# Optimization experiments

Measured on AMD Instinct MI355X. Metric: run time of the kernel, lower is better.

Reference implementation:

```python
import jax, jax.numpy as jnp
import numpy as np

D = 256; NH = 8; NLEV = 4; NPTS = 4; DH = D // NH
DFFN = 1024; B = 8; LQ = 900
SHAPES = np.array([[100, 100], [50, 50], [25, 25], [13, 13]], dtype=np.int64)
STARTS = np.concatenate([[0], np.cumsum(SHAPES[:, 0] * SHAPES[:, 1])[:-1]]).astype(np.int64)
LEN = int((SHAPES[:, 0] * SHAPES[:, 1]).sum())


def _ln(x, w, b, eps=1e-5):
    m = x.mean(-1, keepdims=True)
    v = ((x - m) ** 2).mean(-1, keepdims=True)
    return (x - m) / jnp.sqrt(v + eps) * w + b


def _msdeform(q, ref, src, val_w, val_b, off_w, off_b, aw_w, aw_b, op_w, op_b):
    # Multi-scale deformable attention (Deformable DETR core), grid_sample
    # bilinear / zeros padding / align_corners=False semantics.
    Bq, Lq = q.shape[0], q.shape[1]
    value = (src @ val_w + val_b).reshape(Bq, -1, NH, DH)
    off = (q @ off_w + off_b).reshape(Bq, Lq, NH, NLEV, NPTS, 2)
    aw = jax.nn.softmax((q @ aw_w + aw_b).reshape(Bq, Lq, NH, NLEV * NPTS), -1)
    aw = aw.reshape(Bq, Lq, NH, NLEV, NPTS)
    norm = jnp.asarray(SHAPES[:, ::-1].copy(), dtype=q.dtype)  # (W_l, H_l)
    loc = ref[:, :, None, :, None, :] + off / norm[None, None, None, :, None, :]
    out = jnp.zeros((Bq, Lq, NH, DH), q.dtype)
    for l in range(NLEV):
        Hl, Wl = int(SHAPES[l, 0]), int(SHAPES[l, 1]); s = int(STARTS[l])
        v = value[:, s:s + Hl * Wl]                  # [B, Hl*Wl, NH, DH]
        lx = loc[:, :, :, l, :, 0] * Wl - 0.5        # align_corners=False pixel coords
        ly = loc[:, :, :, l, :, 1] * Hl - 0.5        # [B, Lq, NH, NPTS]
        x0 = jnp.floor(lx); y0 = jnp.floor(ly)
        fx = lx - x0; fy = ly - y0
        x0 = x0.astype(jnp.int32); y0 = y0.astype(jnp.int32)
        samp = jnp.zeros((Bq, Lq, NH, NPTS, DH), q.dtype)
        for dx, dy in ((0, 0), (1, 0), (0, 1), (1, 1)):
            xi = x0 + dx; yi = y0 + dy
            w = (fx if dx else 1.0 - fx) * (fy if dy else 1.0 - fy)
            valid = (xi >= 0) & (xi < Wl) & (yi >= 0) & (yi < Hl)
            idx = jnp.clip(yi, 0, Hl - 1) * Wl + jnp.clip(xi, 0, Wl - 1)
            idx_f = idx.transpose(0, 1, 3, 2).reshape(Bq, Lq * NPTS, NH)
            g = jnp.take_along_axis(v, idx_f[..., None], axis=1)
            g = g.reshape(Bq, Lq, NPTS, NH, DH).transpose(0, 1, 3, 2, 4)
            samp = samp + jnp.where(valid, w, 0.0)[..., None] * g
        out = out + jnp.sum(samp * aw[:, :, :, l, :, None], axis=3)
    return out.reshape(Bq, Lq, D) @ op_w + op_b


def _forward(tgt, query_pos, reference_points, src, qkv_w, qkv_b, out_w, out_b,
             ln2_w, ln2_b, val_w, val_b, off_w, off_b, aw_w, aw_b, op_w, op_b,
             ln1_w, ln1_b, w1, b1, w2, b2, ln3_w, ln3_b):
    Bq, Lq, _ = tgt.shape
    # --- self attention: q=k=tgt+pos, value=tgt (eval mode, no dropout) ---
    q = tgt + query_pos
    wq, wk, wv = qkv_w[:, :D], qkv_w[:, D:2 * D], qkv_w[:, 2 * D:]
    bq, bk, bv = qkv_b[:D], qkv_b[D:2 * D], qkv_b[2 * D:]
    qh = (q @ wq + bq).reshape(Bq, Lq, NH, DH)
    kh = (q @ wk + bk).reshape(Bq, Lq, NH, DH)
    vh = (tgt @ wv + bv).reshape(Bq, Lq, NH, DH)
    scores = jnp.einsum('bqhd,bkhd->bhqk', qh, kh) / jnp.sqrt(jnp.asarray(DH, tgt.dtype))
    attn = jax.nn.softmax(scores, -1)
    sa = jnp.einsum('bhqk,bkhd->bqhd', attn, vh).reshape(Bq, Lq, D) @ out_w + out_b
    tgt = _ln(tgt + sa, ln2_w, ln2_b)
    # --- multi-scale deformable cross attention ---
    ca = _msdeform(tgt + query_pos, reference_points, src,
                   val_w, val_b, off_w, off_b, aw_w, aw_b, op_w, op_b)
    tgt = _ln(tgt + ca, ln1_w, ln1_b)
    # --- FFN ---
    ff = jax.nn.relu(tgt @ w1 + b1) @ w2 + b2
    return _ln(tgt + ff, ln3_w, ln3_b)


def setup_inputs():
    key = jax.random.key(0)
    ks = jax.random.split(key, 16)
    s = 0.02
    return {
        'tgt': jax.random.normal(ks[0], (B, LQ, D), jnp.float32),
        'query_pos': jax.random.normal(ks[1], (B, LQ, D), jnp.float32),
        'reference_points': jax.random.uniform(ks[2], (B, LQ, NLEV, 2), jnp.float32),
        'src': jax.random.normal(ks[3], (B, LEN, D), jnp.float32),
        'spatial_shapes': jnp.asarray(SHAPES),
        'level_start_index': jnp.asarray(STARTS),
        'qkv_w': jax.random.normal(ks[4], (D, 3 * D), jnp.float32) * s,
        'qkv_b': jnp.zeros((3 * D,), jnp.float32),
        'out_w': jax.random.normal(ks[5], (D, D), jnp.float32) * s,
        'out_b': jnp.zeros((D,), jnp.float32),
        'ln2_w': jnp.ones((D,), jnp.float32), 'ln2_b': jnp.zeros((D,), jnp.float32),
        'val_w': jax.random.normal(ks[6], (D, D), jnp.float32) * s,
        'val_b': jnp.zeros((D,), jnp.float32),
        'off_w': jax.random.normal(ks[7], (D, NH * NLEV * NPTS * 2), jnp.float32) * s,
        'off_b': jax.random.normal(ks[8], (NH * NLEV * NPTS * 2,), jnp.float32) * 0.5,
        'aw_w': jax.random.normal(ks[9], (D, NH * NLEV * NPTS), jnp.float32) * s,
        'aw_b': jnp.zeros((NH * NLEV * NPTS,), jnp.float32),
        'op_w': jax.random.normal(ks[10], (D, D), jnp.float32) * s,
        'op_b': jnp.zeros((D,), jnp.float32),
        'ln1_w': jnp.ones((D,), jnp.float32), 'ln1_b': jnp.zeros((D,), jnp.float32),
        'w1': jax.random.normal(ks[11], (D, DFFN), jnp.float32) * s,
        'b1': jnp.zeros((DFFN,), jnp.float32),
        'w2': jax.random.normal(ks[12], (DFFN, D), jnp.float32) * s,
        'b2': jnp.zeros((D,), jnp.float32),
        'ln3_w': jnp.ones((D,), jnp.float32), 'ln3_b': jnp.zeros((D,), jnp.float32),
    }


def reference(tgt, query_pos, reference_points, src, spatial_shapes, level_start_index,
              qkv_w, qkv_b, out_w, out_b, ln2_w, ln2_b, val_w, val_b, off_w, off_b,
              aw_w, aw_b, op_w, op_b, ln1_w, ln1_b, w1, b1, w2, b2, ln3_w, ln3_b):
    return _forward(tgt, query_pos, reference_points, src, qkv_w, qkv_b, out_w, out_b,
                    ln2_w, ln2_b, val_w, val_b, off_w, off_b, aw_w, aw_b, op_w, op_b,
                    ln1_w, ln1_b, w1, b1, w2, b2, ln3_w, ln3_b)
```

## Files before the change

### kernel.cpp

```cpp
#include <hip/hip_runtime.h>
#include <math.h>

#define Dm    256
#define NHm   8
#define DHm   32
#define NLEVm 4
#define NPTSm 4
#define DFFNm 1024
#define Bm    8
#define LQm   900
#define LENm  13294
#define MQ    (Bm * LQm)
#define MV    (Bm * LENm)
#define MQP   7296
#define MVP   106368
#define LQP   960

typedef __attribute__((ext_vector_type(8))) short short8;
typedef __attribute__((ext_vector_type(4))) float f32x4;

__device__ __forceinline__ unsigned short f2bf(float f) {
    unsigned int b = __float_as_uint(f);
    unsigned int r = (b + 0x7FFFu + ((b >> 16) & 1u)) >> 16;
    return (unsigned short)r;
}
__device__ __forceinline__ float bf2f(unsigned short u) {
    return __uint_as_float(((unsigned int)u) << 16);
}

__device__ __forceinline__ void wt_tile(const float* __restrict__ W,
                                        unsigned short* __restrict__ BT,
                                        int N, int K, int n0, int k0, int t,
                                        float (*tile)[65]) {
    #pragma unroll
    for (int r0 = 0; r0 < 64; r0 += 16) {
        int r = r0 + (t >> 4);
        int c = (t & 15) * 4;
        float4 v = *reinterpret_cast<const float4*>(W + (size_t)(k0 + r) * N + n0 + c);
        tile[r][c + 0] = v.x; tile[r][c + 1] = v.y; tile[r][c + 2] = v.z; tile[r][c + 3] = v.w;
    }
    __syncthreads();
    #pragma unroll
    for (int s = t; s < 512; s += 256) {
        int r = s >> 3, c8 = (s & 7) * 8;
        short8 u;
        #pragma unroll
        for (int j = 0; j < 8; ++j) u[j] = (short)f2bf(tile[c8 + j][r]);
        *reinterpret_cast<short8*>(BT + (size_t)(n0 + r) * K + k0 + c8) = u;
    }
}

__global__ __launch_bounds__(256) void wt_prep(
        const float* __restrict__ qkv_w, const float* __restrict__ out_w,
        const float* __restrict__ val_w, const float* __restrict__ off_w,
        const float* __restrict__ aw_w,  const float* __restrict__ op_w,
        const float* __restrict__ w1,    const float* __restrict__ w2,
        unsigned short* __restrict__ BT_qkv, unsigned short* __restrict__ BT_out,
        unsigned short* __restrict__ BT_val, unsigned short* __restrict__ BT_off,
        unsigned short* __restrict__ BT_aw,  unsigned short* __restrict__ BT_op,
        unsigned short* __restrict__ BT_w1,  unsigned short* __restrict__ BT_w2,
        const float* __restrict__ tgt, const float* __restrict__ qpos,
        unsigned short* __restrict__ tgtb, unsigned short* __restrict__ qb) {
    __shared__ float tile[64][65];
    int bid = blockIdx.x;
    int t = threadIdx.x;
    if (bid >= 248) {
        int i = (bid - 248) * 256 + t;
        ushort4 ut, uq;
        if (i < MQ * 64) {
            float4 x = reinterpret_cast<const float4*>(tgt)[i];
            float4 y = reinterpret_cast<const float4*>(qpos)[i];
            ut.x = f2bf(x.x); ut.y = f2bf(x.y); ut.z = f2bf(x.z); ut.w = f2bf(x.w);
            uq.x = f2bf(x.x + y.x); uq.y = f2bf(x.y + y.y);
            uq.z = f2bf(x.z + y.z); uq.w = f2bf(x.w + y.w);
        } else {
            ut.x = ut.y = ut.z = ut.w = 0;
            uq.x = uq.y = uq.z = uq.w = 0;
        }
        reinterpret_cast<ushort4*>(tgtb)[i] = ut;
        reinterpret_cast<ushort4*>(qb)[i] = uq;
        return;
    }
    const float* W; unsigned short* BT; int N, K, idx;
    if      (bid < 48)  { W = qkv_w; BT = BT_qkv; N = 768;  K = 256;  idx = bid; }
    else if (bid < 64)  { W = out_w; BT = BT_out; N = 256;  K = 256;  idx = bid - 48; }
    else if (bid < 80)  { W = val_w; BT = BT_val; N = 256;  K = 256;  idx = bid - 64; }
    else if (bid < 96)  { W = off_w; BT = BT_off; N = 256;  K = 256;  idx = bid - 80; }
    else if (bid < 104) { W = aw_w;  BT = BT_aw;  N = 128;  K = 256;  idx = bid - 96; }
    else if (bid < 120) { W = op_w;  BT = BT_op;  N = 256;  K = 256;  idx = bid - 104; }
    else if (bid < 184) { W = w1;    BT = BT_w1;  N = 1024; K = 256;  idx = bid - 120; }
    else                { W = w2;    BT = BT_w2;  N = 256;  K = 1024; idx = bid - 184; }
    int nt = N / 64;
    int n0 = (idx % nt) * 64, k0 = (idx / nt) * 64;
    wt_tile(W, BT, N, K, n0, k0, t, tile);
}

__device__ __forceinline__ void mfma_tilestep(const unsigned short* Ac, const unsigned short* Bc,
                                              int wr, int wc, int l, f32x4 acc[4][4]) {
    short8 af[4], bfr[4];
    #pragma unroll
    for (int m = 0; m < 4; ++m)
        af[m] = *(const short8*)(Ac + (wr + m * 16 + (l & 15)) * 32 + (l >> 4) * 8);
    #pragma unroll
    for (int n = 0; n < 4; ++n)
        bfr[n] = *(const short8*)(Bc + (wc + n * 16 + (l & 15)) * 32 + (l >> 4) * 8);
    #pragma unroll
    for (int m = 0; m < 4; ++m)
        #pragma unroll
        for (int n = 0; n < 4; ++n)
            acc[m][n] = __builtin_amdgcn_mfma_f32_16x16x32_bf16(af[m], bfr[n], acc[m][n], 0, 0, 0);
}

__device__ __forceinline__ void gemm64_core(int t, unsigned short* Sh,
                                            short8& ra, short8& rb0, short8& rb1,
                                            const unsigned short* ap,
                                            const unsigned short* b0p, const unsigned short* b1p,
                                            const float* afp, f32x4 acc[2][4]) {
    int l = t & 63;
    int lr = l & 15, lg = l >> 4;
    int w = t >> 6;
    int wr = (w >> 1) * 32, wc = (w & 1) * 64;
    unsigned short* As = Sh;
    unsigned short* Bs = Sh + 2048;
    for (int k0 = 0; k0 < 256; k0 += 32) {
        __syncthreads();
        *(short8*)(As + t * 8) = ra;
        *(short8*)(Bs + t * 8) = rb0;
        *(short8*)(Bs + (t + 256) * 8) = rb1;
        __syncthreads();
        if (k0 + 32 < 256) {
            if (afp) {
                float4 f0 = *(const float4*)(afp + k0 + 32);
                float4 f1 = *(const float4*)(afp + k0 + 36);
                ra[0] = (short)f2bf(f0.x); ra[1] = (short)f2bf(f0.y);
                ra[2] = (short)f2bf(f0.z); ra[3] = (short)f2bf(f0.w);
                ra[4] = (short)f2bf(f1.x); ra[5] = (short)f2bf(f1.y);
                ra[6] = (short)f2bf(f1.z); ra[7] = (short)f2bf(f1.w);
            } else {
                ra = *(const short8*)(ap + k0 + 32);
            }
            rb0 = *(const short8*)(b0p + k0 + 32);
            rb1 = *(const short8*)(b1p + k0 + 32);
        }
        short8 af[2], bfr[4];
        #pragma unroll
        for (int m = 0; m < 2; ++m)
            af[m] = *(const short8*)(As + (wr + m * 16 + lr) * 32 + lg * 8);
        #pragma unroll
        for (int n = 0; n < 4; ++n)
            bfr[n] = *(const short8*)(Bs + (wc + n * 16 + lr) * 32 + lg * 8);
        #pragma unroll
        for (int m = 0; m < 2; ++m)
            #pragma unroll
            for (int n = 0; n < 4; ++n)
                acc[m][n] = __builtin_amdgcn_mfma_f32_16x16x32_bf16(af[m], bfr[n], acc[m][n], 0, 0, 0);
    }
}

__device__ __forceinline__ void value_tile64(int vbid, int t, const float* __restrict__ src,
        const unsigned short* __restrict__ BT_val, const float* __restrict__ val_b,
        unsigned short* __restrict__ value_bf, unsigned short* Sh) {
    int l = t & 63, w = t >> 6;
    int lr = l & 15, lg = l >> 4;
    int wr = (w >> 1) * 32, wc = (w & 1) * 64;
    int cr = lg * 4, cc = lr;
    int row0 = (vbid % 1662) * 64, col0 = (vbid / 1662) * 128;
    f32x4 acc[2][4];
    #pragma unroll
    for (int m = 0; m < 2; ++m)
        #pragma unroll
        for (int n = 0; n < 4; ++n) acc[m][n] = (f32x4){0.f, 0.f, 0.f, 0.f};
    int rA = min(row0 + (t >> 2), MV - 1);
    const float* afp = src + (size_t)rA * 256 + (t & 3) * 8;
    const unsigned short* Bg = BT_val + (size_t)col0 * 256;
    const unsigned short* b0p = Bg + (size_t)(t >> 2) * 256 + (t & 3) * 8;
    const unsigned short* b1p = Bg + (size_t)((t + 256) >> 2) * 256 + ((t + 256) & 3) * 8;
    short8 ra, rb0, rb1;
    {
        float4 f0 = *(const float4*)(afp);
        float4 f1 = *(const float4*)(afp + 4);
        ra[0] = (short)f2bf(f0.x); ra[1] = (short)f2bf(f0.y);
        ra[2] = (short)f2bf(f0.z); ra[3] = (short)f2bf(f0.w);
        ra[4] = (short)f2bf(f1.x); ra[5] = (short)f2bf(f1.y);
        ra[6] = (short)f2bf(f1.z); ra[7] = (short)f2bf(f1.w);
    }
    rb0 = *(const short8*)(b0p);
    rb1 = *(const short8*)(b1p);
    gemm64_core(t, Sh, ra, rb0, rb1, nullptr, b0p, b1p, afp, acc);
    #pragma unroll
    for (int m = 0; m < 2; ++m)
        #pragma unroll
        for (int n = 0; n < 4; ++n) {
            int col = col0 + wc + n * 16 + cc;
            float bv = val_b[col];
            #pragma unroll
            for (int j = 0; j < 4; ++j) {
                int r = row0 + wr + m * 16 + cr + j;
                if (r < MV)
                    value_bf[(size_t)r * 256 + col] = f2bf(acc[m][n][j] + bv);
            }
        }
}

__device__ __forceinline__ void flash_block(int sid, int t,
        const unsigned short* __restrict__ qk, const unsigned short* __restrict__ vt,
        unsigned short* __restrict__ out, unsigned short* P_lds ) {
    int l = t & 63, w = t >> 6;
    int lr = l & 15, lg = l >> 4;
    int qt = sid % 15, h = (sid / 15) % 8, b = sid / 120;
    const float scale = 0.17677669529663687f;
    unsigned short* Pw = P_lds + w * 1152;

    short8 qf = *(const short8*)(qk + (size_t)(b * LQm + qt * 64 + w * 16 + lr) * 512 + h * 32 + lg * 8);

    f32x4 accO[2];
    accO[0] = (f32x4){0.f, 0.f, 0.f, 0.f};
    accO[1] = (f32x4){0.f, 0.f, 0.f, 0.f};
    float mrow[4] = {-1e30f, -1e30f, -1e30f, -1e30f};
    float lrow[4] = {0.f, 0.f, 0.f, 0.f};
    const f32x4 zero = (f32x4){0.f, 0.f, 0.f, 0.f};
    const unsigned short* vtb = vt + ((size_t)(b * 256 + h * 32)) * LQP;

    for (int kt = 0; kt < 15; ++kt) {
        int k0 = kt * 64;
        f32x4 sfr[4];
        #pragma unroll
        for (int ks = 0; ks < 4; ++ks) {
            short8 kf = *(const short8*)(qk + (size_t)(b * LQm + k0 + ks * 16 + lr) * 512 + 256 + h * 32 + lg * 8);
            sfr[ks] = __builtin_amdgcn_mfma_f32_16x16x32_bf16(qf, kf, zero, 0, 0, 0);
        }
        float sv[4][4];
        #pragma unroll
        for (int ks = 0; ks < 4; ++ks) {
            bool valid = (k0 + ks * 16 + lr) < LQm;
            #pragma unroll
            for (int j = 0; j < 4; ++j)
                sv[ks][j] = valid ? sfr[ks][j] * scale : -1e30f;
        }
        float tm[4], newm[4], rr[4], ps[4];
        #pragma unroll
        for (int j = 0; j < 4; ++j)
            tm[j] = fmaxf(fmaxf(sv[0][j], sv[1][j]), fmaxf(sv[2][j], sv[3][j]));
        #pragma unroll
        for (int msk = 1; msk <= 8; msk <<= 1) {
            #pragma unroll
            for (int j = 0; j < 4; ++j) tm[j] = fmaxf(tm[j], __shfl_xor(tm[j], msk));
        }
        #pragma unroll
        for (int j = 0; j < 4; ++j) {
            newm[j] = fmaxf(mrow[j], tm[j]);
            rr[j] = __expf(mrow[j] - newm[j]);
            mrow[j] = newm[j];
            ps[j] = 0.f;
        }
        float pv[4][4];
        #pragma unroll
        for (int ks = 0; ks < 4; ++ks)
            #pragma unroll
            for (int j = 0; j < 4; ++j) {
                pv[ks][j] = __expf(sv[ks][j] - newm[j]);
                ps[j] += pv[ks][j];
            }
        #pragma unroll
        for (int msk = 1; msk <= 8; msk <<= 1) {
            #pragma unroll
            for (int j = 0; j < 4; ++j) ps[j] += __shfl_xor(ps[j], msk);
        }
        #pragma unroll
        for (int j = 0; j < 4; ++j) lrow[j] = lrow[j] * rr[j] + ps[j];
        #pragma unroll
        for (int n = 0; n < 2; ++n)
            #pragma unroll
            for (int j = 0; j < 4; ++j) accO[n][j] *= rr[j];
        #pragma unroll
        for (int ks = 0; ks < 4; ++ks)
            #pragma unroll
            for (int j = 0; j < 4; ++j)
                Pw[(lg * 4 + j) * 72 + ks * 16 + lr] = f2bf(pv[ks][j]);
        #pragma unroll
        for (int kh2 = 0; kh2 < 2; ++kh2) {
            short8 pf = *(const short8*)(Pw + lr * 72 + kh2 * 32 + lg * 8);
            #pragma unroll
            for (int n = 0; n < 2; ++n) {
                short8 vf = *(const short8*)(vtb + (size_t)(n * 16 + lr) * LQP + k0 + kh2 * 32 + lg * 8);
                accO[n] = __builtin_amdgcn_mfma_f32_16x16x32_bf16(pf, vf, accO[n], 0, 0, 0);
            }
        }
    }
    float inv[4];
    #pragma unroll
    for (int j = 0; j < 4; ++j) inv[j] = 1.0f / lrow[j];
    #pragma unroll
    for (int n = 0; n < 2; ++n)
        #pragma unroll
        for (int j = 0; j < 4; ++j) {
            int q = qt * 64 + w * 16 + lg * 4 + j;
            if (q < LQm)
                out[(size_t)(b * LQm + q) * 256 + h * 32 + n * 16 + lr] = f2bf(accO[n][j] * inv[j]);
        }
}

__global__ __launch_bounds__(256) void qkvt_kernel(
        const unsigned short* __restrict__ Qbf, const unsigned short* __restrict__ BT_qkv,
        const float* __restrict__ qkv_b, unsigned short* __restrict__ qk_bf,
        const unsigned short* __restrict__ tgt_bf, unsigned short* __restrict__ Vt) {
    __shared__ __align__(16) unsigned short Sh[6144];
    int bid = blockIdx.x;
    int t = threadIdx.x;
    if (bid >= 684) {
        int i = (bid - 684) * 256 + t;
        int row = i / 60, c = 900 + (i % 60);
        Vt[(size_t)row * LQP + c] = 0;
        return;
    }
    int l = t & 63, w = t >> 6;
    int lr = l & 15, lg = l >> 4;
    int wr = (w >> 1) * 32, wc = (w & 1) * 64;
    int cr = lg * 4, cc = lr;
    f32x4 acc[2][4];
    #pragma unroll
    for (int m = 0; m < 2; ++m)
        #pragma unroll
        for (int n = 0; n < 4; ++n) acc[m][n] = (f32x4){0.f, 0.f, 0.f, 0.f};

    bool is_qk = (bid < 456);
    int idx = is_qk ? bid : (bid - 456);
    int row0 = (idx % 114) * 64;
    int col0 = (idx / 114) * 128;
    const unsigned short* A  = is_qk ? Qbf : tgt_bf;
    const unsigned short* BT = is_qk ? BT_qkv : (BT_qkv + 512 * 256);
    const float* bias        = is_qk ? qkv_b : (qkv_b + 512);
    const unsigned short* ap  = A  + (size_t)(row0 + (t >> 2)) * 256 + (t & 3) * 8;
    const unsigned short* Bg  = BT + (size_t)col0 * 256;
    const unsigned short* b0p = Bg + (size_t)(t >> 2) * 256 + (t & 3) * 8;
    const unsigned short* b1p = Bg + (size_t)((t + 256) >> 2) * 256 + ((t + 256) & 3) * 8;
    short8 ra = *(const short8*)(ap);
    short8 rb0 = *(const short8*)(b0p);
    short8 rb1 = *(const short8*)(b1p);
    gemm64_core(t, Sh, ra, rb0, rb1, ap, b0p, b1p, nullptr, acc);
    if (is_qk) {
        #pragma unroll
        for (int m = 0; m < 2; ++m)
            #pragma unroll
            for (int n = 0; n < 4; ++n) {
                int col = col0 + wc + n * 16 + cc;
                float bv = bias[col];
                #pragma unroll
                for (int j = 0; j < 4; ++j) {
                    int r = row0 + wr + m * 16 + cr + j;
                    if (r < MQ)
                        qk_bf[(size_t)r * 512 + col] = f2bf(acc[m][n][j] + bv);
                }
            }
    } else {
        #pragma unroll
        for (int m = 0; m < 2; ++m)
            #pragma unroll
            for (int n = 0; n < 4; ++n) {
                int col = col0 + wc + n * 16 + cc;
                float bv = bias[col];
                int r0 = row0 + wr + m * 16 + cr;
                if (r0 < MQ) {
                    int bb = r0 / 900;
                    int q = r0 - bb * 900;
                    ushort4 u;
                    u.x = f2bf(acc[m][n][0] + bv);
                    u.y = f2bf(acc[m][n][1] + bv);
                    u.z = f2bf(acc[m][n][2] + bv);
                    u.w = f2bf(acc[m][n][3] + bv);
                    *reinterpret_cast<ushort4*>(Vt + ((size_t)(bb * 256 + col)) * LQP + q) = u;
                }
            }
    }
}

__global__ __launch_bounds__(256) void flash_value(
        const unsigned short* __restrict__ qk_bf, const unsigned short* __restrict__ Vt,
        unsigned short* __restrict__ attn_bf,
        const float* __restrict__ src, const unsigned short* __restrict__ BT_val,
        const float* __restrict__ val_b, unsigned short* __restrict__ value_bf) {
    __shared__ __align__(16) unsigned short Sh[6144];
    int bid = blockIdx.x;
    int t = threadIdx.x;
    if (bid < 960) {
        flash_block(bid, t, qk_bf, Vt, attn_bf, Sh);
    } else {
        value_tile64(bid - 960, t, src, BT_val, val_b, value_bf, Sh);
    }
}

template <int RELU, int OBF>
__global__ __launch_bounds__(256) void bgemm(int M, int N, int K,
        const unsigned short* __restrict__ A,
        const unsigned short* __restrict__ BT,
        const float* __restrict__ bias, const float* __restrict__ bias2,
        float* __restrict__ Cf, float* __restrict__ Cf2,
        unsigned short* __restrict__ Cb, int ldc) {
    __shared__ __align__(16) unsigned short As[2][128 * 32];
    __shared__ __align__(16) unsigned short Bs[2][128 * 32];
    int t = threadIdx.x;
    int l = t & 63;
    int w = t >> 6;
    int row0 = blockIdx.x * 128, col0 = blockIdx.y * 128;
    int wr = (w >> 1) * 64, wc = (w & 1) * 64;
    f32x4 acc[4][4];
    #pragma unroll
    for (int m = 0; m < 4; ++m)
        #pragma unroll
        for (int n = 0; n < 4; ++n) acc[m][n] = (f32x4){0.f, 0.f, 0.f, 0.f};

    int s0 = t, s1 = t + 256;
    const unsigned short* Ag = A + (size_t)row0 * K;
    const unsigned short* Bg = BT + (size_t)col0 * K;
    const unsigned short* a0p = Ag + (size_t)(s0 >> 2) * K + (s0 & 3) * 8;
    const unsigned short* a1p = Ag + (size_t)(s1 >> 2) * K + (s1 & 3) * 8;
    const unsigned short* b0p = Bg + (size_t)(s0 >> 2) * K + (s0 & 3) * 8;
    const unsigned short* b1p = Bg + (size_t)(s1 >> 2) * K + (s1 & 3) * 8;

    short8 ra0 = *(const short8*)(a0p);
    short8 ra1 = *(const short8*)(a1p);
    short8 rb0 = *(const short8*)(b0p);
    short8 rb1 = *(const short8*)(b1p);

    int cur = 0;
    for (int k0 = 0; k0 < K; k0 += 32) {
        unsigned short* Ac = As[cur];
        unsigned short* Bc = Bs[cur];
        *(short8*)(Ac + s0 * 8) = ra0;
        *(short8*)(Ac + s1 * 8) = ra1;
        *(short8*)(Bc + s0 * 8) = rb0;
        *(short8*)(Bc + s1 * 8) = rb1;
        if (k0 + 32 < K) {
            ra0 = *(const short8*)(a0p + k0 + 32);
            ra1 = *(const short8*)(a1p + k0 + 32);
            rb0 = *(const short8*)(b0p + k0 + 32);
            rb1 = *(const short8*)(b1p + k0 + 32);
        }
        __syncthreads();
        mfma_tilestep(Ac, Bc, wr, wc, l, acc);
        cur ^= 1;
    }

    int cr = (l >> 4) * 4;
    int cc = l & 15;
    #pragma unroll
    for (int m = 0; m < 4; ++m) {
        #pragma unroll
        for (int n = 0; n < 4; ++n) {
            int col = col0 + wc + n * 16 + cc;
            if (OBF == 3) {
                float bv = (col < 256) ? bias[col] : bias2[col - 256];
                #pragma unroll
                for (int j = 0; j < 4; ++j) {
                    int r = row0 + wr + m * 16 + cr + j;
                    if (r < M) {
                        float v = acc[m][n][j] + bv;
                        if (col < 256) Cf[(size_t)r * 256 + col] = v;
                        else           Cf2[(size_t)r * 128 + (col - 256)] = v;
                    }
                }
            } else {
                float bv = bias[col];
                #pragma unroll
                for (int j = 0; j < 4; ++j) {
                    int r = row0 + wr + m * 16 + cr + j;
                    if (r < M) {
                        float v = acc[m][n][j] + bv;
                        if (RELU) v = fmaxf(v, 0.f);
                        if (OBF) Cb[(size_t)r * ldc + col] = f2bf(v);
                        else     Cf[(size_t)r * ldc + col] = v;
                    }
                }
            }
        }
    }
}

template <int DUAL, int QP>
__global__ __launch_bounds__(256) void add_ln_kernel(const float* __restrict__ x,
                                                     const float* __restrict__ r,
                                                     const float* __restrict__ w,
                                                     const float* __restrict__ b,
                                                     const float* __restrict__ qpos,
                                                     float* __restrict__ out,
                                                     unsigned short* __restrict__ outb,
                                                     unsigned short* __restrict__ outq) {
    int row = blockIdx.x * 4 + (threadIdx.x >> 6);
    int lane = threadIdx.x & 63;
    size_t i4 = (size_t)row * 64 + lane;
    float4 xv = reinterpret_cast<const float4*>(x)[i4];
    float4 rv = reinterpret_cast<const float4*>(r)[i4];
    float4 v = make_float4(xv.x + rv.x, xv.y + rv.y, xv.z + rv.z, xv.w + rv.w);
    float s = v.x + v.y + v.z + v.w;
    #pragma unroll
    for (int msk = 1; msk <= 32; msk <<= 1) s += __shfl_xor(s, msk);
    float mean = s * (1.0f / Dm);
    float4 dv = make_float4(v.x - mean, v.y - mean, v.z - mean, v.w - mean);
    float sq = dv.x * dv.x + dv.y * dv.y + dv.z * dv.z + dv.w * dv.w;
    #pragma unroll
    for (int msk = 1; msk <= 32; msk <<= 1) sq += __shfl_xor(sq, msk);
    float is = rsqrtf(sq * (1.0f / Dm) + 1e-5f);
    float4 wv = reinterpret_cast<const float4*>(w)[lane];
    float4 bv = reinterpret_cast<const float4*>(b)[lane];
    float4 res = make_float4(dv.x * is * wv.x + bv.x, dv.y * is * wv.y + bv.y,
                             dv.z * is * wv.z + bv.z, dv.w * is * wv.w + bv.w);
    reinterpret_cast<float4*>(out)[i4] = res;
    if (DUAL) {
        ushort4 u;
        u.x = f2bf(res.x); u.y = f2bf(res.y); u.z = f2bf(res.z); u.w = f2bf(res.w);
        reinterpret_cast<ushort4*>(outb)[i4] = u;
    }
    if (QP) {
        float4 qv = reinterpret_cast<const float4*>(qpos)[i4];
        ushort4 u;
        u.x = f2bf(res.x + qv.x); u.y = f2bf(res.y + qv.y);
        u.z = f2bf(res.z + qv.z); u.w = f2bf(res.w + qv.w);
        reinterpret_cast<ushort4*>(outq)[i4] = u;
    }
}

__global__ __launch_bounds__(256) void msdeform_kernel(const unsigned short* __restrict__ value,
                                                       const float* __restrict__ ref,
                                                       const float* __restrict__ off,
                                                       const float* __restrict__ awl,
                                                       unsigned short* __restrict__ out) {
    const int HL[4] = {100, 50, 25, 13};
    const int ST[4] = {0, 10000, 12500, 13125};
    __shared__ float lsx[4][128], lsy[4][128], wtab[4][128];
    __shared__ float2 ctab[4][512];
    int wv = threadIdx.x >> 6, lane = threadIdx.x & 63;
    int m = blockIdx.x * 4 + wv;
    int b = m / LQm;

    #pragma unroll
    for (int e = lane; e < 128; e += 64) {
        int lev = (e >> 2) & 3;
        float rx = ref[((size_t)m * NLEVm + lev) * 2 + 0];
        float ry = ref[((size_t)m * NLEVm + lev) * 2 + 1];
        float ox = off[(size_t)m * 256 + e * 2 + 0];
        float oy = off[(size_t)m * 256 + e * 2 + 1];
        float Wf = (float)HL[lev];
        lsx[wv][e] = (rx + ox / Wf) * Wf - 0.5f;
        lsy[wv][e] = (ry + oy / Wf) * Wf - 0.5f;
        wtab[wv][e] = awl[(size_t)m * 128 + e];
    }
    __syncthreads();
    if (lane < NHm) {
        int h = lane;
        float mx = -1e30f;
        #pragma unroll
        for (int i = 0; i < 16; i++) mx = fmaxf(mx, wtab[wv][h * 16 + i]);
        float s = 0.f;
        #pragma unroll
        for (int i = 0; i < 16; i++) {
            float e = __expf(wtab[wv][h * 16 + i] - mx);
            wtab[wv][h * 16 + i] = e; s += e;
        }
        float inv = 1.0f / s;
        #pragma unroll
        for (int i = 0; i < 16; i++) wtab[wv][h * 16 + i] *= inv;
    }
    __syncthreads();
    #pragma unroll
    for (int j = 0; j < 8; ++j) {
        int e2 = lane * 8 + j;
        int c = e2 & 3, e = e2 >> 2;
        int lev = (e >> 2) & 3;
        int Wl = HL[lev];
        float lx = lsx[wv][e], ly = lsy[wv][e];
        float x0f = floorf(lx), y0f = floorf(ly);
        float fx = lx - x0f, fy = ly - y0f;
        int dx = c & 1, dy = c >> 1;
        int xi = (int)x0f + dx, yi = (int)y0f + dy;
        bool valid = (xi >= 0) && (xi < Wl) && (yi >= 0) && (yi < Wl);
        float wc = valid ? ((dx ? fx : 1.0f - fx) * (dy ? fy : 1.0f - fy)) * wtab[wv][e] : 0.f;
        int xc = min(max(xi, 0), Wl - 1), yc = min(max(yi, 0), Wl - 1);
        int row = b * LENm + ST[lev] + yc * Wl + xc;
        ctab[wv][e2] = make_float2(__int_as_float(row), wc);
    }
    __syncthreads();
    int h = lane >> 3, dg = lane & 7;
    const unsigned short* basep = value + h * 32 + dg * 4;
    float a0 = 0.f, a1 = 0.f, a2 = 0.f, a3 = 0.f;
    #pragma unroll
    for (int i = 0; i < 16; ++i) {
        #pragma unroll
        for (int c = 0; c < 4; ++c) {
            float2 cc = ctab[wv][(h * 16 + i) * 4 + c];
            int row = __float_as_int(cc.x);
            float wc = cc.y;
            ushort4 v = *reinterpret_cast<const ushort4*>(basep + (size_t)row * 256);
            a0 += wc * bf2f(v.x); a1 += wc * bf2f(v.y);
            a2 += wc * bf2f(v.z); a3 += wc * bf2f(v.w);
        }
    }
    ushort4 o;
    o.x = f2bf(a0); o.y = f2bf(a1); o.z = f2bf(a2); o.w = f2bf(a3);
    *reinterpret_cast<ushort4*>(out + (size_t)m * 256 + h * 32 + dg * 4) = o;
}

extern "C" void kernel_launch(void* const* d_in, const int* in_sizes, int n_in,
                              void* d_out, int out_size, void* d_ws, size_t ws_size,
                              hipStream_t stream) {
    const float* tgt   = (const float*)d_in[0];
    const float* qpos  = (const float*)d_in[1];
    const float* refp  = (const float*)d_in[2];
    const float* src   = (const float*)d_in[3];
    const float* qkv_w = (const float*)d_in[6];
    const float* qkv_b = (const float*)d_in[7];
    const float* out_w = (const float*)d_in[8];
    const float* out_b = (const float*)d_in[9];
    const float* ln2_w = (const float*)d_in[10];
    const float* ln2_b = (const float*)d_in[11];
    const float* val_w = (const float*)d_in[12];
    const float* val_b = (const float*)d_in[13];
    const float* off_w = (const float*)d_in[14];
    const float* off_b = (const float*)d_in[15];
    const float* aw_w  = (const float*)d_in[16];
    const float* aw_b  = (const float*)d_in[17];
    const float* op_w  = (const float*)d_in[18];
    const float* op_b  = (const float*)d_in[19];
    const float* ln1_w = (const float*)d_in[20];
    const float* ln1_b = (const float*)d_in[21];
    const float* w1    = (const float*)d_in[22];
    const float* b1    = (const float*)d_in[23];
    const float* w2    = (const float*)d_in[24];
    const float* b2    = (const float*)d_in[25];
    const float* ln3_w = (const float*)d_in[26];
    const float* ln3_b = (const float*)d_in[27];

    char* base = (char*)d_ws;
    unsigned short* value_bf  = (unsigned short*)(base);
    unsigned short* hidden_bf = (unsigned short*)(base + 54460416);
    unsigned short* t2_bf     = (unsigned short*)(base + 54460416 + 14942208);
    unsigned short* qk_bf = (unsigned short*)(base + 108920832);
    float* offb = (float*)(base + 108920832);
    float* awb  = (float*)(base + 108920832 + 7372800);
    unsigned short* Vt = (unsigned short*)(base + 123666432);
    float* S1   = (float*)(base + 123666432);
    float* t1   = (float*)(base + 131039232);
    float* t2   = (float*)(base + 138412032);
    unsigned short* Qbf     = (unsigned short*)(base + 145784832);
    unsigned short* tgt_bf  = (unsigned short*)(base + 149520384);
    unsigned short* attn_bf = (unsigned short*)(base + 153255936);
    unsigned short* ca_bf   = (unsigned short*)(base + 156991488);
    unsigned short* BT_qkv  = (unsigned short*)(base + 160727040);
    unsigned short* BT_out  = BT_qkv + 768 * 256;
    unsigned short* BT_val  = BT_out + 256 * 256;
    unsigned short* BT_off  = BT_val + 256 * 256;
    unsigned short* BT_aw   = BT_off + 256 * 256;
    unsigned short* BT_op   = BT_aw + 128 * 256;
    unsigned short* BT_w1   = BT_op + 256 * 256;
    unsigned short* BT_w2   = BT_w1 + 1024 * 256;
    float* outp = (float*)d_out;

    dim3 blk(256);
    wt_prep<<<dim3(2072), blk, 0, stream>>>(qkv_w, out_w, val_w, off_w, aw_w, op_w, w1, w2,
                                            BT_qkv, BT_out, BT_val, BT_off, BT_aw, BT_op, BT_w1, BT_w2,
                                            tgt, qpos, tgt_bf, Qbf);
    qkvt_kernel<<<dim3(1164), blk, 0, stream>>>(Qbf, BT_qkv, qkv_b, qk_bf, tgt_bf, Vt);
    flash_value<<<dim3(4284), blk, 0, stream>>>(qk_bf, Vt, attn_bf, src, BT_val, val_b, value_bf);
    bgemm<0, 0><<<dim3(57, 2), blk, 0, stream>>>(MQ, 256, 256, attn_bf, BT_out, out_b, nullptr, S1, nullptr, nullptr, 256);
    add_ln_kernel<0, 1><<<dim3(1800), blk, 0, stream>>>(tgt, S1, ln2_w, ln2_b, qpos, t1, nullptr, Qbf);
    bgemm<0, 3><<<dim3(57, 3), blk, 0, stream>>>(MQ, 384, 256, Qbf, BT_off, off_b, aw_b, offb, awb, nullptr, 0);
    msdeform_kernel<<<dim3(1800), blk, 0, stream>>>(value_bf, refp, offb, awb, ca_bf);
    bgemm<0, 0><<<dim3(57, 2), blk, 0, stream>>>(MQ, 256, 256, ca_bf, BT_op, op_b, nullptr, S1, nullptr, nullptr, 256);
    add_ln_kernel<1, 0><<<dim3(1800), blk, 0, stream>>>(t1, S1, ln1_w, ln1_b, nullptr, t2, t2_bf, nullptr);
    bgemm<1, 1><<<dim3(57, 8), blk, 0, stream>>>(MQ, DFFNm, 256, t2_bf, BT_w1, b1, nullptr, nullptr, nullptr, hidden_bf, DFFNm);
    bgemm<0, 0><<<dim3(57, 2), blk, 0, stream>>>(MQ, 256, 1024, hidden_bf, BT_w2, b2, nullptr, S1, nullptr, nullptr, 256);
    add_ln_kernel<0, 0><<<dim3(1800), blk, 0, stream>>>(t2, S1, ln3_w, ln3_b, nullptr, outp, nullptr, nullptr);
}
```

Baseline: 239.7 us.

## Fuse output-projection GEMMs with residual add and LayerNorm epilogue

Adds a bgemm_ln kernel in which each 64-row block computes all 256 output columns. It then adds the bias and the residual and applies LayerNorm in the epilogue, with a cross-wave shared-memory reduction for the row statistics. This replaces three GEMM plus add_ln kernel pairs, removing the fp32 S1 intermediate round trip and three launches. In exchange the grid drops to 113 blocks, which may underuse the GPU's CUs. The variance uses E[x²]−mean², which is less numerically stable, and the GEMM loop is single-buffered with small tiles.

```diff
diff --git a/kernel.cpp b/kernel.cpp
--- a/kernel.cpp
+++ b/kernel.cpp
@@ -389,6 +389,136 @@
     }
 }
 
+template <int VAR>
+__global__ __launch_bounds__(256) void bgemm_ln(int K,
+        const unsigned short* __restrict__ A,
+        const unsigned short* __restrict__ BT,
+        const float* __restrict__ bias,
+        const float* __restrict__ x,
+        const float* __restrict__ lnw, const float* __restrict__ lnb,
+        const float* __restrict__ qpos,
+        float* __restrict__ outf, unsigned short* __restrict__ outb) {
+    __shared__ __align__(16) unsigned short As[64 * 32];
+    __shared__ __align__(16) unsigned short Bs[256 * 32];
+    __shared__ float red[4][64][2];
+    int t = threadIdx.x;
+    int l = t & 63, w = t >> 6;
+    int lr = l & 15, lg = l >> 4;
+    int row0 = blockIdx.x * 64;
+
+    f32x4 acc[4][4];
+    #pragma unroll
+    for (int m = 0; m < 4; ++m)
+        #pragma unroll
+        for (int n = 0; n < 4; ++n) acc[m][n] = (f32x4){0.f, 0.f, 0.f, 0.f};
+
+    const unsigned short* ap = A + (size_t)(row0 + (t >> 2)) * K + (t & 3) * 8;
+    const unsigned short* bp[4];
+    #pragma unroll
+    for (int i = 0; i < 4; ++i) {
+        int s = i * 256 + t;
+        bp[i] = BT + (size_t)(s >> 2) * K + (s & 3) * 8;
+    }
+    short8 ra = *(const short8*)(ap);
+    short8 rb[4];
+    #pragma unroll
+    for (int i = 0; i < 4; ++i) rb[i] = *(const short8*)(bp[i]);
+
+    for (int k0 = 0; k0 < K; k0 += 32) {
+        __syncthreads();
+        *(short8*)(As + t * 8) = ra;
+        #pragma unroll
+        for (int i = 0; i < 4; ++i)
+            *(short8*)(Bs + (i * 256 + t) * 8) = rb[i];
+        __syncthreads();
+        if (k0 + 32 < K) {
+            ra = *(const short8*)(ap + k0 + 32);
+            #pragma unroll
+            for (int i = 0; i < 4; ++i) rb[i] = *(const short8*)(bp[i] + k0 + 32);
+        }
+        short8 af[4], bfr[4];
+        #pragma unroll
+        for (int m = 0; m < 4; ++m)
+            af[m] = *(const short8*)(As + (m * 16 + lr) * 32 + lg * 8);
+        #pragma unroll
+        for (int n = 0; n < 4; ++n)
+            bfr[n] = *(const short8*)(Bs + (w * 64 + n * 16 + lr) * 32 + lg * 8);
+        #pragma unroll
+        for (int m = 0; m < 4; ++m)
+            #pragma unroll
+            for (int n = 0; n < 4; ++n)
+                acc[m][n] = __builtin_amdgcn_mfma_f32_16x16x32_bf16(af[m], bfr[n], acc[m][n], 0, 0, 0);
+    }
+
+    float bvn[4];
+    #pragma unroll
+    for (int n = 0; n < 4; ++n) bvn[n] = bias[w * 64 + n * 16 + lr];
+    #pragma unroll
+    for (int m = 0; m < 4; ++m)
+        #pragma unroll
+        for (int j = 0; j < 4; ++j) {
+            int row = row0 + m * 16 + lg * 4 + j;
+            if (row < MQ) {
+                #pragma unroll
+                for (int n = 0; n < 4; ++n)
+                    acc[m][n][j] += bvn[n] + x[(size_t)row * 256 + w * 64 + n * 16 + lr];
+            }
+        }
+    #pragma unroll
+    for (int m = 0; m < 4; ++m)
+        #pragma unroll
+        for (int j = 0; j < 4; ++j) {
+            float s = 0.f, q = 0.f;
+            #pragma unroll
+            for (int n = 0; n < 4; ++n) {
+                float v = acc[m][n][j];
+                s += v; q += v * v;
+            }
+            #pragma unroll
+            for (int msk = 1; msk <= 8; msk <<= 1) {
+                s += __shfl_xor(s, msk);
+                q += __shfl_xor(q, msk);
+            }
+            if (lr == 0) {
+                int rowloc = m * 16 + lg * 4 + j;
+                red[w][rowloc][0] = s;
+                red[w][rowloc][1] = q;
+            }
+        }
+    __syncthreads();
+    float lnwv[4], lnbv[4];
+    #pragma unroll
+    for (int n = 0; n < 4; ++n) {
+        lnwv[n] = lnw[w * 64 + n * 16 + lr];
+        lnbv[n] = lnb[w * 64 + n * 16 + lr];
+    }
+    #pragma unroll
+    for (int m = 0; m < 4; ++m)
+        #pragma unroll
+        for (int j = 0; j < 4; ++j) {
+            int rowloc = m * 16 + lg * 4 + j;
+            int row = row0 + rowloc;
+            if (row >= MQ) continue;
+            float tot  = red[0][rowloc][0] + red[1][rowloc][0] + red[2][rowloc][0] + red[3][rowloc][0];
+            float totq = red[0][rowloc][1] + red[1][rowloc][1] + red[2][rowloc][1] + red[3][rowloc][1];
+            float mean = tot * (1.0f / 256.0f);
+            float var  = totq * (1.0f / 256.0f) - mean * mean;
+            float is   = rsqrtf(var + 1e-5f);
+            #pragma unroll
+            for (int n = 0; n < 4; ++n) {
+                int col = w * 64 + n * 16 + lr;
+                float res = (acc[m][n][j] - mean) * is * lnwv[n] + lnbv[n];
+                outf[(size_t)row * 256 + col] = res;
+                if (VAR == 0) {
+                    float qv = qpos[(size_t)row * 256 + col];
+                    outb[(size_t)row * 256 + col] = f2bf(res + qv);
+                } else if (VAR == 1) {
+                    outb[(size_t)row * 256 + col] = f2bf(res);
+                }
+            }
+        }
+}
+
 template <int RELU, int OBF>
 __global__ __launch_bounds__(256) void bgemm(int M, int N, int K,
         const unsigned short* __restrict__ A,
@@ -467,55 +597,11 @@
                     if (r < M) {
                         float v = acc[m][n][j] + bv;
                         if (RELU) v = fmaxf(v, 0.f);
-                        if (OBF) Cb[(size_t)r * ldc + col] = f2bf(v);
-                        else     Cf[(size_t)r * ldc + col] = v;
+                        Cb[(size_t)r * ldc + col] = f2bf(v);
                     }
                 }
             }
         }
-    }
-}
-
-template <int DUAL, int QP>
-__global__ __launch_bounds__(256) void add_ln_kernel(const float* __restrict__ x,
-                                                     const float* __restrict__ r,
-                                                     const float* __restrict__ w,
-                                                     const float* __restrict__ b,
-                                                     const float* __restrict__ qpos,
-                                                     float* __restrict__ out,
-                                                     unsigned short* __restrict__ outb,
-                                                     unsigned short* __restrict__ outq) {
-    int row = blockIdx.x * 4 + (threadIdx.x >> 6);
-    int lane = threadIdx.x & 63;
-    size_t i4 = (size_t)row * 64 + lane;
-    float4 xv = reinterpret_cast<const float4*>(x)[i4];
-    float4 rv = reinterpret_cast<const float4*>(r)[i4];
-    float4 v = make_float4(xv.x + rv.x, xv.y + rv.y, xv.z + rv.z, xv.w + rv.w);
-    float s = v.x + v.y + v.z + v.w;
-    #pragma unroll
-    for (int msk = 1; msk <= 32; msk <<= 1) s += __shfl_xor(s, msk);
-    float mean = s * (1.0f / Dm);
-    float4 dv = make_float4(v.x - mean, v.y - mean, v.z - mean, v.w - mean);
-    float sq = dv.x * dv.x + dv.y * dv.y + dv.z * dv.z + dv.w * dv.w;
-    #pragma unroll
-    for (int msk = 1; msk <= 32; msk <<= 1) sq += __shfl_xor(sq, msk);
-    float is = rsqrtf(sq * (1.0f / Dm) + 1e-5f);
-    float4 wv = reinterpret_cast<const float4*>(w)[lane];
-    float4 bv = reinterpret_cast<const float4*>(b)[lane];
-    float4 res = make_float4(dv.x * is * wv.x + bv.x, dv.y * is * wv.y + bv.y,
-                             dv.z * is * wv.z + bv.z, dv.w * is * wv.w + bv.w);
-    reinterpret_cast<float4*>(out)[i4] = res;
-    if (DUAL) {
-        ushort4 u;
-        u.x = f2bf(res.x); u.y = f2bf(res.y); u.z = f2bf(res.z); u.w = f2bf(res.w);
-        reinterpret_cast<ushort4*>(outb)[i4] = u;
-    }
-    if (QP) {
-        float4 qv = reinterpret_cast<const float4*>(qpos)[i4];
-        ushort4 u;
-        u.x = f2bf(res.x + qv.x); u.y = f2bf(res.y + qv.y);
-        u.z = f2bf(res.z + qv.z); u.w = f2bf(res.w + qv.w);
-        reinterpret_cast<ushort4*>(outq)[i4] = u;
     }
 }
 
@@ -637,7 +723,6 @@
     float* offb = (float*)(base + 108920832);
     float* awb  = (float*)(base + 108920832 + 7372800);
     unsigned short* Vt = (unsigned short*)(base + 123666432);
-    float* S1   = (float*)(base + 123666432);
     float* t1   = (float*)(base + 131039232);
     float* t2   = (float*)(base + 138412032);
     unsigned short* Qbf     = (unsigned short*)(base + 145784832);
@@ -660,13 +745,13 @@
                                             tgt, qpos, tgt_bf, Qbf);
     qkvt_kernel<<<dim3(1164), blk, 0, stream>>>(Qbf, BT_qkv, qkv_b, qk_bf, tgt_bf, Vt);
     flash_value<<<dim3(4284), blk, 0, stream>>>(qk_bf, Vt, attn_bf, src, BT_val, val_b, value_bf);
-    bgemm<0, 0><<<dim3(57, 2), blk, 0, stream>>>(MQ, 256, 256, attn_bf, BT_out, out_b, nullptr, S1, nullptr, nullptr, 256);
-    add_ln_kernel<0, 1><<<dim3(1800), blk, 0, stream>>>(tgt, S1, ln2_w, ln2_b, qpos, t1, nullptr, Qbf);
+    bgemm_ln<0><<<dim3(113), blk, 0, stream>>>(256, attn_bf, BT_out, out_b, tgt,
+                                               ln2_w, ln2_b, qpos, t1, Qbf);
     bgemm<0, 3><<<dim3(57, 3), blk, 0, stream>>>(MQ, 384, 256, Qbf, BT_off, off_b, aw_b, offb, awb, nullptr, 0);
     msdeform_kernel<<<dim3(1800), blk, 0, stream>>>(value_bf, refp, offb, awb, ca_bf);
-    bgemm<0, 0><<<dim3(57, 2), blk, 0, stream>>>(MQ, 256, 256, ca_bf, BT_op, op_b, nullptr, S1, nullptr, nullptr, 256);
-    add_ln_kernel<1, 0><<<dim3(1800), blk, 0, stream>>>(t1, S1, ln1_w, ln1_b, nullptr, t2, t2_bf, nullptr);
+    bgemm_ln<1><<<dim3(113), blk, 0, stream>>>(256, ca_bf, BT_op, op_b, t1,
+                                               ln1_w, ln1_b, nullptr, t2, t2_bf);
     bgemm<1, 1><<<dim3(57, 8), blk, 0, stream>>>(MQ, DFFNm, 256, t2_bf, BT_w1, b1, nullptr, nullptr, nullptr, hidden_bf, DFFNm);
-    bgemm<0, 0><<<dim3(57, 2), blk, 0, stream>>>(MQ, 256, 1024, hidden_bf, BT_w2, b2, nullptr, S1, nullptr, nullptr, 256);
-    add_ln_kernel<0, 0><<<dim3(1800), blk, 0, stream>>>(t2, S1, ln3_w, ln3_b, nullptr, outp, nullptr, nullptr);
-}
+    bgemm_ln<2><<<dim3(113), blk, 0, stream>>>(1024, hidden_bf, BT_w2, b2, t2,
+                                               ln3_w, ln3_b, nullptr, outp, nullptr);
+}
```

Measured after the change: 252.2 us. +5.2%, slower.
